# Kernel optimization log

Hardware: AMD Instinct MI355X
Metric: run time of the kernel (lower is better)

Reference implementation:

```python
import jax, jax.numpy as jnp
import numpy as np

B, C, H, W = 4, 128, 96, 96
OC = 128          # out_channels
K = 3             # kernel_size
OFF = 2 * K * K   # offset channels = 18
PAD = 1
EPS = 1e-6


def conv2d(x, w, b, pad=1, groups=1):
    out = jax.lax.conv_general_dilated(
        x, w, window_strides=(1, 1), padding=[(pad, pad), (pad, pad)],
        dimension_numbers=('NCHW', 'OIHW', 'NCHW'), feature_group_count=groups)
    return out + b[None, :, None, None]


def bilinear_gather(x, ys, xs):
    # x: [B,C,H,W]; ys, xs: [B,H,W] float sample coords. Zero outside bounds.
    Bn, Cn, Hn, Wn = x.shape
    xflat = x.reshape(Bn, Cn, Hn * Wn)
    y0 = jnp.floor(ys)
    x0 = jnp.floor(xs)
    out = jnp.zeros((Bn, Cn, Hn, Wn), dtype=x.dtype)
    for dy, dx in ((0, 0), (0, 1), (1, 0), (1, 1)):
        yy = y0 + dy
        xx = x0 + dx
        w = (1.0 - jnp.abs(ys - yy)) * (1.0 - jnp.abs(xs - xx))
        valid = (yy >= 0) & (yy < Hn) & (xx >= 0) & (xx < Wn)
        yi = jnp.clip(yy, 0, Hn - 1).astype(jnp.int32)
        xi = jnp.clip(xx, 0, Wn - 1).astype(jnp.int32)
        idx = (yi * Wn + xi).reshape(Bn, 1, Hn * Wn)
        g = jnp.take_along_axis(xflat, idx, axis=2).reshape(Bn, Cn, Hn, Wn)
        out = out + (w * valid)[:, None] * g
    return out


def deform_conv(x, offsets, w, b):
    # torchvision DeformConv2d v1: offsets [B, 2*K*K, H, W], pairs (dy, dx) per tap
    Bn, Cn, Hn, Wn = x.shape
    off = offsets.reshape(Bn, K * K, 2, Hn, Wn)
    gy, gx = jnp.meshgrid(jnp.arange(Hn, dtype=x.dtype),
                          jnp.arange(Wn, dtype=x.dtype), indexing='ij')
    acc = jnp.zeros((Bn, w.shape[0], Hn, Wn), dtype=x.dtype)
    for k in range(K * K):
        ky, kx = k // K, k % K
        ys = gy[None] - PAD + ky + off[:, k, 0]
        xs = gx[None] - PAD + kx + off[:, k, 1]
        samp = bilinear_gather(x, ys, xs)                 # [B,C,H,W]
        acc = acc + jnp.einsum('bchw,oc->bohw', samp, w[:, :, ky, kx])
    return acc + b[None, :, None, None]


def setup_inputs() -> dict:
    key = jax.random.key(0)
    ks = jax.random.split(key, 8)
    s = 0.05
    return {
        'x': jax.random.normal(ks[0], (B, C, H, W), jnp.float32),
        'w_off': jax.random.normal(ks[1], (OFF, C, K, K), jnp.float32) * s,
        'b_off': jnp.zeros((OFF,), jnp.float32),
        'w_def': jax.random.normal(ks[2], (OC, C, K, K), jnp.float32) * s,
        'b_def': jnp.zeros((OC,), jnp.float32),
        'ln_w': jnp.ones((OC,), jnp.float32),
        'ln_b': jnp.zeros((OC,), jnp.float32),
        'w_dw': jax.random.normal(ks[3], (C, 1, 3, 3), jnp.float32) * s,
        'b_dw': jnp.zeros((C,), jnp.float32),
        'w_pw': jax.random.normal(ks[4], (OC, C, 1, 1), jnp.float32) * s,
        'b_pw': jnp.zeros((OC,), jnp.float32),
    }


def reference(x, w_off, b_off, w_def, b_def, ln_w, ln_b, w_dw, b_dw, w_pw, b_pw):
    offsets = conv2d(x, w_off, b_off, pad=PAD)            # [B,18,H,W]
    x1 = deform_conv(x, offsets, w_def, b_def)            # [B,OC,H,W]
    # channels-first LayerNorm
    u = x1.mean(1, keepdims=True)
    s = ((x1 - u) ** 2).mean(1, keepdims=True)
    x1 = ln_w[None, :, None, None] * ((x1 - u) / jnp.sqrt(s + EPS)) \
         + ln_b[None, :, None, None]
    x2 = conv2d(x, w_dw, b_dw, pad=1, groups=C)           # depthwise 3x3
    x4 = conv2d(x2 + x, w_pw, b_pw, pad=0)                # pointwise 1x1
    x4 = jax.nn.silu(x4)
    return x1 + x4
```

## Files before the change

### kernel.cpp

```cpp
#include <hip/hip_runtime.h>
#include <hip/hip_bf16.h>
#include <stdint.h>

#define BN 4
#define CN 128
#define HN 96
#define WN 96
#define HW (HN*WN)
#define OCN 128
#define OFFC 18
#define EPSV 1e-6f
#define HP 98
#define WP 98

typedef __attribute__((ext_vector_type(8))) short bf16x8;
typedef __attribute__((ext_vector_type(4))) float f32x4;

__device__ __forceinline__ float lo16(uint32_t u) {
  union { uint32_t i; float f; } v; v.i = u << 16; return v.f;
}
__device__ __forceinline__ float hi16(uint32_t u) {
  union { uint32_t i; float f; } v; v.i = u & 0xffff0000u; return v.f;
}
__device__ __forceinline__ uint16_t f2b(float f) {
  union { float f; uint32_t i; } u; u.f = f;
  uint32_t r = u.i + 0x7fffu + ((u.i >> 16) & 1u);
  return (uint16_t)(r >> 16);
}
__device__ __forceinline__ uint32_t pk2(float a, float b) {
  return (uint32_t)f2b(a) | ((uint32_t)f2b(b) << 16);
}
__device__ __forceinline__ int swz(int row, int c) { return c ^ ((row & 7) << 3); }

__device__ __align__(16) uint16_t g_def[9 * 128 * 128];
__device__ __align__(16) uint16_t g_pw[128 * 128];
__device__ __align__(16) uint16_t g_off[32 * 1152];
__device__ __align__(16) uint16_t g_xp[(size_t)BN * HP * WP * CN];

__global__ __launch_bounds__(256)
void k_prep_w(const float* __restrict__ w_def, const float* __restrict__ w_pw,
              const float* __restrict__ w_off) {
  int i = blockIdx.x * 256 + threadIdx.x;
  if (i < 147456) {
    int k = i >> 14, rem = i & 16383, oc = rem >> 7, c = rem & 127;
    g_def[i] = f2b(w_def[((oc << 7) + c) * 9 + k]);
  } else if (i < 147456 + 16384) {
    int j = i - 147456;
    g_pw[j] = f2b(w_pw[j]);
  } else if (i < 147456 + 16384 + 36864) {
    int j = i - 163840;
    int row = j / 1152, col = j - row * 1152;
    int kk = col >> 7, c = col & 127;
    g_off[j] = (row < OFFC) ? f2b(w_off[((row << 7) + c) * 9 + kk]) : (uint16_t)0;
  }
}

__global__ __launch_bounds__(256)
void k_prep_x(const float* __restrict__ x) {
  __shared__ uint16_t trans[96][136];
  int blk = blockIdx.x;
  int y1 = blk % HP;
  int b  = blk / HP;
  int t = (int)threadIdx.x;
  uint16_t* dst = g_xp + ((size_t)(b * HP + y1) * WP) * CN;
  if (y1 == 0 || y1 == HP - 1) {
    for (int i = t; i < WP * CN / 8; i += 256)
      ((uint4*)dst)[i] = make_uint4(0, 0, 0, 0);
    return;
  }
  int y = y1 - 1;
  for (int i = t; i < CN * WN / 4; i += 256) {
    int c = i / 24, xq = i - c * 24;
    float4 f = *(const float4*)&x[((size_t)(b * CN + c) * HN + y) * WN + xq * 4];
    trans[xq * 4 + 0][c] = f2b(f.x);
    trans[xq * 4 + 1][c] = f2b(f.y);
    trans[xq * 4 + 2][c] = f2b(f.z);
    trans[xq * 4 + 3][c] = f2b(f.w);
  }
  __syncthreads();
  for (int i = t; i < 2 * CN / 8; i += 256) {
    int side = i >> 4, j = i & 15;
    ((uint4*)(dst + (size_t)side * (WP - 1) * CN))[j] = make_uint4(0, 0, 0, 0);
  }
  for (int i = t; i < WN * CN / 8; i += 256) {
    int xw = i >> 4, cq = (i & 15) * 8;
    ((uint4*)(dst + CN))[i] = *(const uint4*)&trans[xw][cq];
  }
}

__global__ __launch_bounds__(256, 4)
void k_fused(const float* __restrict__ b_off, const float* __restrict__ b_def,
             const float* __restrict__ ln_w, const float* __restrict__ ln_b,
             const float* __restrict__ w_dw, const float* __restrict__ b_dw,
             const float* __restrict__ b_pw, float* __restrict__ out) {
  __shared__ __align__(16) uint16_t patch[3 * 34 * 128];
  __shared__ float offarena[576];
  float (*offl)[32] = (float (*)[32])offarena;
  float (*red1)[32] = (float (*)[32])offarena;
  float (*red2)[32] = (float (*)[32])(offarena + 128);
  float* muv = offarena + 256;
  float* rsv = offarena + 288;
  uint16_t* samp0 = patch;
  uint16_t* samp1 = patch + 4096;
  uint16_t* dwT   = patch + 8192;

  int bid = blockIdx.x;
  int wid = (bid & 7) * 144 + (bid >> 3);
  int wt = wid % 3;
  int h  = (wid / 3) % HN;
  int b  = wid / (3 * HN);
  int w0 = wt * 32;

  int t = (int)threadIdx.x;
  int l = t & 63, w = t >> 6;
  int g = l >> 4, fr = l & 15;
  int p = t & 31, cg = t >> 5;
  const uint16_t* xb = g_xp + (size_t)b * HP * WP * CN;
  int cbase = w * 32 + (l & 3) * 8;
  const uint16_t* bp = xb + cbase;

  #pragma unroll
  for (int rep = 0; rep < 7; ++rep) {
    int e = t + 256 * rep;
    if (e < 1632) {
      int rec = e >> 4, chunk = e & 15;
      int ky = rec / 34, i = rec - 34 * ky;
      const uint16_t* src = xb + ((size_t)(h + ky) * WP + (w0 + i)) * CN + chunk * 8;
      *(uint4*)&patch[((ky * 34 + i) << 7) + swz(i, chunk * 8)] = *(const uint4*)src;
    }
  }
  __syncthreads();

  {
    int toc = w >> 1, tp = w & 1;
    f32x4 aco = {0.f, 0.f, 0.f, 0.f};
    #pragma unroll
    for (int ks = 0; ks < 36; ++ks) {
      int kk = ks >> 2;
      int ky = kk / 3, kx = kk - 3 * ky;
      int cb = ((ks & 3) << 5) + (g << 3);
      int i = fr + (tp << 4) + kx;
      bf16x8 a = *(const bf16x8*)&g_off[(toc * 16 + fr) * 1152 + (ks << 5) + (g << 3)];
      bf16x8 bb = *(const bf16x8*)&patch[((ky * 34 + i) << 7) + swz(i, cb)];
      aco = __builtin_amdgcn_mfma_f32_16x16x32_bf16(a, bb, aco, 0, 0, 0);
    }
    #pragma unroll
    for (int reg = 0; reg < 4; ++reg) {
      int j = toc * 16 + g * 4 + reg;
      if (j < OFFC) offl[j][(tp << 4) + fr] = aco[reg] + b_off[j];
    }
  }

  float adw[16];
  {
    #pragma unroll
    for (int cl = 0; cl < 16; ++cl) adw[cl] = b_dw[cg * 16 + cl];
    #pragma unroll
    for (int ky = 0; ky < 3; ++ky) {
      #pragma unroll
      for (int kx = 0; kx < 3; ++kx) {
        int i = p + kx;
        uint32_t r[8];
        *(uint4*)&r[0] = *(const uint4*)&patch[((ky * 34 + i) << 7) + swz(i, cg * 16)];
        *(uint4*)&r[4] = *(const uint4*)&patch[((ky * 34 + i) << 7) + swz(i, cg * 16 + 8)];
        #pragma unroll
        for (int c2 = 0; c2 < 8; ++c2) {
          adw[2 * c2]     += lo16(r[c2]) * w_dw[(cg * 16 + 2 * c2) * 9 + ky * 3 + kx];
          adw[2 * c2 + 1] += hi16(r[c2]) * w_dw[(cg * 16 + 2 * c2 + 1) * 9 + ky * 3 + kx];
        }
      }
    }
    int i = p + 1;
    uint32_t r[8];
    *(uint4*)&r[0] = *(const uint4*)&patch[((34 + i) << 7) + swz(i, cg * 16)];
    *(uint4*)&r[4] = *(const uint4*)&patch[((34 + i) << 7) + swz(i, cg * 16 + 8)];
    #pragma unroll
    for (int c2 = 0; c2 < 8; ++c2) {
      adw[2 * c2]     += lo16(r[c2]);
      adw[2 * c2 + 1] += hi16(r[c2]);
    }
  }
  __syncthreads();

  auto GATHER = [&](int kk, uint16_t* wb) {
    int ky = kk / 3, kx = kk - 3 * ky;
    #pragma unroll
    for (int half = 0; half < 2; ++half) {
      int px = half * 16 + (l >> 2);
      float dy = offl[2 * kk][px], dx = offl[2 * kk + 1][px];
      float ys = (float)(h - 1 + ky) + dy;
      float xs = (float)(w0 + px - 1 + kx) + dx;
      float y0f = floorf(ys), x0f = floorf(xs);
      float fy = ys - y0f, fx = xs - x0f;
      int y0 = (int)y0f, x0 = (int)x0f;
      float w00 = (1.f - fy) * (1.f - fx), w01 = (1.f - fy) * fx;
      float w10 = fy * (1.f - fx),         w11 = fy * fx;
      bool yok0 = (y0 >= 0) & (y0 < HN), yok1 = (y0 + 1 >= 0) & (y0 + 1 < HN);
      bool xok0 = (x0 >= 0) & (x0 < WN), xok1 = (x0 + 1 >= 0) & (x0 + 1 < WN);
      if (!(yok0 & xok0)) w00 = 0.f;
      if (!(yok0 & xok1)) w01 = 0.f;
      if (!(yok1 & xok0)) w10 = 0.f;
      if (!(yok1 & xok1)) w11 = 0.f;
      int ya  = min(max(y0, -1), HN) + 1;
      int yb2 = min(max(y0 + 1, -1), HN) + 1;
      int xa  = min(max(x0, -1), WN) + 1;
      int xc2 = min(max(x0 + 1, -1), WN) + 1;
      uint32_t A[4], B[4], C[4], D[4];
      *(uint4*)A = *(const uint4*)(bp + ((size_t)ya * WP + xa) * CN);
      *(uint4*)B = *(const uint4*)(bp + ((size_t)ya * WP + xc2) * CN);
      *(uint4*)C = *(const uint4*)(bp + ((size_t)yb2 * WP + xa) * CN);
      *(uint4*)D = *(const uint4*)(bp + ((size_t)yb2 * WP + xc2) * CN);
      uint32_t pk4[4];
      #pragma unroll
      for (int q2 = 0; q2 < 4; ++q2) {
        float s0 = w00 * lo16(A[q2]) + w01 * lo16(B[q2]) + w10 * lo16(C[q2]) + w11 * lo16(D[q2]);
        float s1 = w00 * hi16(A[q2]) + w01 * hi16(B[q2]) + w10 * hi16(C[q2]) + w11 * hi16(D[q2]);
        pk4[q2] = pk2(s0, s1);
      }
      *(uint4*)&wb[(px << 7) + swz(px, cbase)] = *(uint4*)pk4;
    }
  };

  {
    #pragma unroll
    for (int m = 0; m < 2; ++m) {
      uint4 u = { pk2(adw[8*m+0], adw[8*m+1]), pk2(adw[8*m+2], adw[8*m+3]),
                  pk2(adw[8*m+4], adw[8*m+5]), pk2(adw[8*m+6], adw[8*m+7]) };
      *(uint4*)&dwT[(p << 7) + swz(p, cg * 16 + 8 * m)] = u;
    }
    GATHER(0, samp0);
  }
  __syncthreads();

  f32x4 a4[2][2];
  #pragma unroll
  for (int q1 = 0; q1 < 2; ++q1)
    #pragma unroll
    for (int q2 = 0; q2 < 2; ++q2) a4[q1][q2] = (f32x4){0.f, 0.f, 0.f, 0.f};
  {
    #pragma unroll
    for (int ks = 0; ks < 4; ++ks) {
      int kb = (ks << 5) + (g << 3);
      bf16x8 a0 = *(const bf16x8*)&g_pw[(32 * w + fr) * 128 + kb];
      bf16x8 a1 = *(const bf16x8*)&g_pw[(32 * w + 16 + fr) * 128 + kb];
      #pragma unroll
      for (int tp2 = 0; tp2 < 2; ++tp2) {
        int pp = (tp2 << 4) + fr;
        bf16x8 bb = *(const bf16x8*)&dwT[(pp << 7) + swz(pp, kb)];
        a4[0][tp2] = __builtin_amdgcn_mfma_f32_16x16x32_bf16(a0, bb, a4[0][tp2], 0, 0, 0);
        a4[1][tp2] = __builtin_amdgcn_mfma_f32_16x16x32_bf16(a1, bb, a4[1][tp2], 0, 0, 0);
      }
    }
    #pragma unroll
    for (int toc2 = 0; toc2 < 2; ++toc2)
      #pragma unroll
      for (int tp2 = 0; tp2 < 2; ++tp2)
        #pragma unroll
        for (int reg = 0; reg < 4; ++reg) {
          int oc = 32 * w + 16 * toc2 + 4 * g + reg;
          float v = a4[toc2][tp2][reg] + b_pw[oc];
          a4[toc2][tp2][reg] = v / (1.f + __expf(-v));
        }
  }
  __syncthreads();

  f32x4 ac1[2][2];
  #pragma unroll
  for (int q1 = 0; q1 < 2; ++q1)
    #pragma unroll
    for (int q2 = 0; q2 < 2; ++q2) ac1[q1][q2] = (f32x4){0.f, 0.f, 0.f, 0.f};

  #pragma unroll 1
  for (int k = 0; k < 9; ++k) {
    uint16_t* rb = (k & 1) ? samp1 : samp0;
    uint16_t* wb = (k & 1) ? samp0 : samp1;
    if (k < 8) GATHER(k + 1, wb);
    {
      const uint16_t* gdk = g_def + (k << 14);
      #pragma unroll
      for (int ks = 0; ks < 4; ++ks) {
        int kb = (ks << 5) + (g << 3);
        bf16x8 a0 = *(const bf16x8*)&gdk[(32 * w + fr) * 128 + kb];
        bf16x8 a1 = *(const bf16x8*)&gdk[(32 * w + 16 + fr) * 128 + kb];
        #pragma unroll
        for (int tp2 = 0; tp2 < 2; ++tp2) {
          int pp = (tp2 << 4) + fr;
          bf16x8 bb = *(const bf16x8*)&rb[(pp << 7) + swz(pp, kb)];
          ac1[0][tp2] = __builtin_amdgcn_mfma_f32_16x16x32_bf16(a0, bb, ac1[0][tp2], 0, 0, 0);
          ac1[1][tp2] = __builtin_amdgcn_mfma_f32_16x16x32_bf16(a1, bb, ac1[1][tp2], 0, 0, 0);
        }
      }
    }
    __syncthreads();
  }

  #pragma unroll
  for (int toc2 = 0; toc2 < 2; ++toc2)
    #pragma unroll
    for (int tp2 = 0; tp2 < 2; ++tp2)
      #pragma unroll
      for (int reg = 0; reg < 4; ++reg) {
        int oc = 32 * w + 16 * toc2 + 4 * g + reg;
        ac1[toc2][tp2][reg] += b_def[oc];
      }
  {
    float s1[2], s2[2];
    #pragma unroll
    for (int tp2 = 0; tp2 < 2; ++tp2) {
      float a = 0.f, q = 0.f;
      #pragma unroll
      for (int toc2 = 0; toc2 < 2; ++toc2)
        #pragma unroll
        for (int reg = 0; reg < 4; ++reg) {
          float v = ac1[toc2][tp2][reg];
          a += v; q += v * v;
        }
      a += __shfl_xor(a, 16); a += __shfl_xor(a, 32);
      q += __shfl_xor(q, 16); q += __shfl_xor(q, 32);
      s1[tp2] = a; s2[tp2] = q;
    }
    if (l < 16) {
      red1[w][l] = s1[0]; red1[w][l + 16] = s1[1];
      red2[w][l] = s2[0]; red2[w][l + 16] = s2[1];
    }
  }
  __syncthreads();
  if (t < 32) {
    float m = (red1[0][t] + red1[1][t] + red1[2][t] + red1[3][t]) * (1.f / 128.f);
    float q = (red2[0][t] + red2[1][t] + red2[2][t] + red2[3][t]) * (1.f / 128.f) - m * m;
    muv[t] = m;
    rsv[t] = rsqrtf(q + EPSV);
  }
  __syncthreads();
  {
    #pragma unroll
    for (int toc2 = 0; toc2 < 2; ++toc2)
      #pragma unroll
      for (int tp2 = 0; tp2 < 2; ++tp2) {
        int pp = (tp2 << 4) + fr;
        float mm = muv[pp], rr = rsv[pp];
        #pragma unroll
        for (int reg = 0; reg < 4; ++reg) {
          int oc = 32 * w + 16 * toc2 + 4 * g + reg;
          float v = (ac1[toc2][tp2][reg] - mm) * rr * ln_w[oc] + ln_b[oc]
                    + a4[toc2][tp2][reg];
          out[((size_t)(b * OCN + oc) * HN + h) * WN + w0 + pp] = v;
        }
      }
  }
}

extern "C" void kernel_launch(void* const* d_in, const int* in_sizes, int n_in,
                              void* d_out, int out_size, void* d_ws, size_t ws_size,
                              hipStream_t stream) {
  const float* x     = (const float*)d_in[0];
  const float* w_off = (const float*)d_in[1];
  const float* b_off = (const float*)d_in[2];
  const float* w_def = (const float*)d_in[3];
  const float* b_def = (const float*)d_in[4];
  const float* ln_w  = (const float*)d_in[5];
  const float* ln_b  = (const float*)d_in[6];
  const float* w_dw  = (const float*)d_in[7];
  const float* b_dw  = (const float*)d_in[8];
  const float* w_pw  = (const float*)d_in[9];
  const float* b_pw  = (const float*)d_in[10];
  float* out = (float*)d_out;

  hipLaunchKernelGGL(k_prep_w, dim3(784), dim3(256), 0, stream, w_def, w_pw, w_off);
  hipLaunchKernelGGL(k_prep_x, dim3(BN * HP), dim3(256), 0, stream, x);
  hipLaunchKernelGGL(k_fused, dim3(BN * HN * 3), dim3(256), 0, stream,
                     b_off, b_def, ln_w, ln_b, w_dw, b_dw, b_pw, out);
}
```

Before: 117.3 us.

## Split fused kernel into separate gather and GEMM kernels via global buffers

Breaks the fused kernel into two launches. k_gather computes offsets, the depthwise conv and all nine bilinear-sampled taps, and writes them as bf16 into large global buffers. k_gemm stages those tiles into LDS with double buffering and runs the MFMA GEMMs, LayerNorm and SiLU. The intent is to decouple the latency-bound gather from the MFMA work so each kernel gets its own occupancy. The cost is about 9x the activation volume written to and read back from HBM (roughly 100+ MB of traffic), plus an extra launch.

```diff
diff --git a/kernel.cpp b/kernel.cpp
--- a/kernel.cpp
+++ b/kernel.cpp
@@ -12,6 +12,7 @@
 #define EPSV 1e-6f
 #define HP 98
 #define WP 98
+#define NWG (BN*HN*3)
 
 typedef __attribute__((ext_vector_type(8))) short bf16x8;
 typedef __attribute__((ext_vector_type(4))) float f32x4;
@@ -36,6 +37,8 @@
 __device__ __align__(16) uint16_t g_pw[128 * 128];
 __device__ __align__(16) uint16_t g_off[32 * 1152];
 __device__ __align__(16) uint16_t g_xp[(size_t)BN * HP * WP * CN];
+__device__ __align__(16) uint16_t g_samp[(size_t)9 * BN * HW * CN];
+__device__ __align__(16) uint16_t g_dw[(size_t)BN * HW * CN];
 
 __global__ __launch_bounds__(256)
 void k_prep_w(const float* __restrict__ w_def, const float* __restrict__ w_pw,
@@ -88,21 +91,11 @@
   }
 }
 
-__global__ __launch_bounds__(256, 4)
-void k_fused(const float* __restrict__ b_off, const float* __restrict__ b_def,
-             const float* __restrict__ ln_w, const float* __restrict__ ln_b,
-             const float* __restrict__ w_dw, const float* __restrict__ b_dw,
-             const float* __restrict__ b_pw, float* __restrict__ out) {
+__global__ __launch_bounds__(256, 2)
+void k_gather(const float* __restrict__ b_off, const float* __restrict__ w_dw,
+              const float* __restrict__ b_dw) {
   __shared__ __align__(16) uint16_t patch[3 * 34 * 128];
-  __shared__ float offarena[576];
-  float (*offl)[32] = (float (*)[32])offarena;
-  float (*red1)[32] = (float (*)[32])offarena;
-  float (*red2)[32] = (float (*)[32])(offarena + 128);
-  float* muv = offarena + 256;
-  float* rsv = offarena + 288;
-  uint16_t* samp0 = patch;
-  uint16_t* samp1 = patch + 4096;
-  uint16_t* dwT   = patch + 8192;
+  __shared__ float offl[OFFC][32];
 
   int bid = blockIdx.x;
   int wid = (bid & 7) * 144 + (bid >> 3);
@@ -151,8 +144,8 @@
     }
   }
 
-  float adw[16];
   {
+    float adw[16];
     #pragma unroll
     for (int cl = 0; cl < 16; ++cl) adw[cl] = b_dw[cg * 16 + cl];
     #pragma unroll
@@ -179,11 +172,18 @@
       adw[2 * c2]     += lo16(r[c2]);
       adw[2 * c2 + 1] += hi16(r[c2]);
     }
-  }
-  __syncthreads();
-
-  auto GATHER = [&](int kk, uint16_t* wb) {
+    uint16_t* dd = g_dw + ((size_t)b * HW + h * WN + w0 + p) * CN + cg * 16;
+    *(uint4*)dd       = make_uint4(pk2(adw[0], adw[1]), pk2(adw[2], adw[3]),
+                                   pk2(adw[4], adw[5]), pk2(adw[6], adw[7]));
+    *(uint4*)(dd + 8) = make_uint4(pk2(adw[8], adw[9]), pk2(adw[10], adw[11]),
+                                   pk2(adw[12], adw[13]), pk2(adw[14], adw[15]));
+  }
+  __syncthreads();
+
+  #pragma unroll 1
+  for (int kk = 0; kk < 9; ++kk) {
     int ky = kk / 3, kx = kk - 3 * ky;
+    uint16_t* sd = g_samp + (((size_t)kk * BN + b) * HW + h * WN + w0) * CN;
     #pragma unroll
     for (int half = 0; half < 2; ++half) {
       int px = half * 16 + (l >> 2);
@@ -217,19 +217,68 @@
         float s1 = w00 * hi16(A[q2]) + w01 * hi16(B[q2]) + w10 * hi16(C[q2]) + w11 * hi16(D[q2]);
         pk4[q2] = pk2(s0, s1);
       }
-      *(uint4*)&wb[(px << 7) + swz(px, cbase)] = *(uint4*)pk4;
+      *(uint4*)(sd + (size_t)px * CN + cbase) = *(uint4*)pk4;
+    }
+  }
+}
+
+__global__ __launch_bounds__(256, 4)
+void k_gemm(const float* __restrict__ b_def,
+            const float* __restrict__ ln_w, const float* __restrict__ ln_b,
+            const float* __restrict__ b_pw, float* __restrict__ out) {
+  __shared__ __align__(16) uint16_t s0buf[4096], s1buf[4096], dwT[4096];
+  __shared__ float redarena[576];
+  float (*red1)[32] = (float (*)[32])redarena;
+  float (*red2)[32] = (float (*)[32])(redarena + 128);
+  float* muv = redarena + 256;
+  float* rsv = redarena + 288;
+
+  int bid = blockIdx.x;
+  int wid = (bid & 7) * 144 + (bid >> 3);
+  int wt = wid % 3;
+  int h  = (wid / 3) % HN;
+  int b  = wid / (3 * HN);
+  int w0 = wt * 32;
+
+  int t = (int)threadIdx.x;
+  int l = t & 63, w = t >> 6;
+  int g = l >> 4, fr = l & 15;
+
+  size_t pixbase = (size_t)b * HW + h * WN + w0;
+
+  auto STAGE = [&](const uint16_t* src, uint16_t* dst) {
+    #pragma unroll
+    for (int r = 0; r < 2; ++r) {
+      int e = t + 256 * r;
+      int px = e >> 4, chunk = e & 15;
+      *(uint4*)&dst[(px << 7) + swz(px, chunk * 8)] = *(const uint4*)(src + e * 8);
     }
   };
 
-  {
-    #pragma unroll
-    for (int m = 0; m < 2; ++m) {
-      uint4 u = { pk2(adw[8*m+0], adw[8*m+1]), pk2(adw[8*m+2], adw[8*m+3]),
-                  pk2(adw[8*m+4], adw[8*m+5]), pk2(adw[8*m+6], adw[8*m+7]) };
-      *(uint4*)&dwT[(p << 7) + swz(p, cg * 16 + 8 * m)] = u;
-    }
-    GATHER(0, samp0);
-  }
+  f32x4 ac1[2][2];
+  #pragma unroll
+  for (int q1 = 0; q1 < 2; ++q1)
+    #pragma unroll
+    for (int q2 = 0; q2 < 2; ++q2) ac1[q1][q2] = (f32x4){0.f, 0.f, 0.f, 0.f};
+  auto TAPMM = [&](int k, const uint16_t* rb) {
+    const uint16_t* gdk = g_def + (k << 14);
+    #pragma unroll
+    for (int ks = 0; ks < 4; ++ks) {
+      int kb = (ks << 5) + (g << 3);
+      bf16x8 a0 = *(const bf16x8*)&gdk[(32 * w + fr) * 128 + kb];
+      bf16x8 a1 = *(const bf16x8*)&gdk[(32 * w + 16 + fr) * 128 + kb];
+      #pragma unroll
+      for (int tp2 = 0; tp2 < 2; ++tp2) {
+        int pp = (tp2 << 4) + fr;
+        bf16x8 bb = *(const bf16x8*)&rb[(pp << 7) + swz(pp, kb)];
+        ac1[0][tp2] = __builtin_amdgcn_mfma_f32_16x16x32_bf16(a0, bb, ac1[0][tp2], 0, 0, 0);
+        ac1[1][tp2] = __builtin_amdgcn_mfma_f32_16x16x32_bf16(a1, bb, ac1[1][tp2], 0, 0, 0);
+      }
+    }
+  };
+
+  STAGE(g_dw + pixbase * CN, dwT);
+  STAGE(g_samp + ((size_t)0 * BN * HW + pixbase) * CN, s0buf);
   __syncthreads();
 
   f32x4 a4[2][2];
@@ -237,6 +286,7 @@
   for (int q1 = 0; q1 < 2; ++q1)
     #pragma unroll
     for (int q2 = 0; q2 < 2; ++q2) a4[q1][q2] = (f32x4){0.f, 0.f, 0.f, 0.f};
+  STAGE(g_samp + ((size_t)1 * BN * HW + pixbase) * CN, s1buf);
   {
     #pragma unroll
     for (int ks = 0; ks < 4; ++ks) {
@@ -251,6 +301,7 @@
         a4[1][tp2] = __builtin_amdgcn_mfma_f32_16x16x32_bf16(a1, bb, a4[1][tp2], 0, 0, 0);
       }
     }
+    TAPMM(0, s0buf);
     #pragma unroll
     for (int toc2 = 0; toc2 < 2; ++toc2)
       #pragma unroll
@@ -264,33 +315,12 @@
   }
   __syncthreads();
 
-  f32x4 ac1[2][2];
-  #pragma unroll
-  for (int q1 = 0; q1 < 2; ++q1)
-    #pragma unroll
-    for (int q2 = 0; q2 < 2; ++q2) ac1[q1][q2] = (f32x4){0.f, 0.f, 0.f, 0.f};
-
   #pragma unroll 1
-  for (int k = 0; k < 9; ++k) {
-    uint16_t* rb = (k & 1) ? samp1 : samp0;
-    uint16_t* wb = (k & 1) ? samp0 : samp1;
-    if (k < 8) GATHER(k + 1, wb);
-    {
-      const uint16_t* gdk = g_def + (k << 14);
-      #pragma unroll
-      for (int ks = 0; ks < 4; ++ks) {
-        int kb = (ks << 5) + (g << 3);
-        bf16x8 a0 = *(const bf16x8*)&gdk[(32 * w + fr) * 128 + kb];
-        bf16x8 a1 = *(const bf16x8*)&gdk[(32 * w + 16 + fr) * 128 + kb];
-        #pragma unroll
-        for (int tp2 = 0; tp2 < 2; ++tp2) {
-          int pp = (tp2 << 4) + fr;
-          bf16x8 bb = *(const bf16x8*)&rb[(pp << 7) + swz(pp, kb)];
-          ac1[0][tp2] = __builtin_amdgcn_mfma_f32_16x16x32_bf16(a0, bb, ac1[0][tp2], 0, 0, 0);
-          ac1[1][tp2] = __builtin_amdgcn_mfma_f32_16x16x32_bf16(a1, bb, ac1[1][tp2], 0, 0, 0);
-        }
-      }
-    }
+  for (int k = 1; k < 9; ++k) {
+    uint16_t* rb = (k & 1) ? s1buf : s0buf;
+    uint16_t* wb = (k & 1) ? s0buf : s1buf;
+    if (k < 8) STAGE(g_samp + ((size_t)(k + 1) * BN * HW + pixbase) * CN, wb);
+    TAPMM(k, rb);
     __syncthreads();
   }
 
@@ -368,6 +398,7 @@
 
   hipLaunchKernelGGL(k_prep_w, dim3(784), dim3(256), 0, stream, w_def, w_pw, w_off);
   hipLaunchKernelGGL(k_prep_x, dim3(BN * HP), dim3(256), 0, stream, x);
-  hipLaunchKernelGGL(k_fused, dim3(BN * HN * 3), dim3(256), 0, stream,
-                     b_off, b_def, ln_w, ln_b, w_dw, b_dw, b_pw, out);
-}
+  hipLaunchKernelGGL(k_gather, dim3(NWG), dim3(256), 0, stream, b_off, w_dw, b_dw);
+  hipLaunchKernelGGL(k_gemm, dim3(NWG), dim3(256), 0, stream,
+                     b_def, ln_w, ln_b, b_pw, out);
+}
```

Measured after the change: 138.5 us. 1.18x slower.
